# Performance work log

Measured on AMD Instinct MI355X. Metric: run time of the kernel, lower is better.

Reference implementation:

```python
import jax, jax.numpy as jnp
import numpy as np

B, T, TRAIN = 4, 2048, 1536
D, H, L, FF, V = 512, 8, 12, 2048, 100
DH = D // H
ROPE_BASE = 100000.0


def layer_norm(x, g, b, eps=1e-5):
    mu = jnp.mean(x, axis=-1, keepdims=True)
    var = jnp.mean(jnp.square(x - mu), axis=-1, keepdims=True)
    return (x - mu) * jax.lax.rsqrt(var + eps) * g + b


def rope_cos_sin(t, dh):
    inv_freq = 1.0 / (ROPE_BASE ** (jnp.arange(0, dh, 2, dtype=jnp.float32) / dh))  # (dh/2,)
    ang = jnp.arange(t, dtype=jnp.float32)[:, None] * inv_freq[None, :]  # (T, dh/2)
    return jnp.cos(ang), jnp.sin(ang)


def apply_rope_interleaved(x, cos, sin):
    # x: (B, T, H, DH); interleaved pairs (x0,x1),(x2,x3),...
    x1, x2 = x[..., 0::2], x[..., 1::2]
    c, s = cos[None, :, None, :], sin[None, :, None, :]
    r1 = x1 * c - x2 * s
    r2 = x1 * s + x2 * c
    return jnp.stack([r1, r2], axis=-1).reshape(x.shape)


def setup_inputs() -> dict:
    key = jax.random.key(0)
    ks = jax.random.split(key, 20)
    sc = 0.02
    inp = {
        'R': jax.random.normal(ks[0], (B, T, D), jnp.float32),
        'y_train': jax.random.randint(ks[1], (B, TRAIN), 0, V),
        'emb': jax.random.normal(ks[2], (V, D), jnp.float32) * sc,
        'Wqkv': jax.random.normal(ks[3], (L, D, 3 * D), jnp.float32) * sc,
        'bqkv': jnp.zeros((L, 3 * D), jnp.float32),
        'Wo': jax.random.normal(ks[4], (L, D, D), jnp.float32) * sc,
        'bo': jnp.zeros((L, D), jnp.float32),
        'ln1_g': jnp.ones((L, D), jnp.float32),
        'ln1_b': jnp.zeros((L, D), jnp.float32),
        'ln2_g': jnp.ones((L, D), jnp.float32),
        'ln2_b': jnp.zeros((L, D), jnp.float32),
        'W1': jax.random.normal(ks[5], (L, D, FF), jnp.float32) * sc,
        'b1': jnp.zeros((L, FF), jnp.float32),
        'W2': jax.random.normal(ks[6], (L, FF, D), jnp.float32) * sc,
        'b2': jnp.zeros((L, D), jnp.float32),
        'pW1': jax.random.normal(ks[7], (D, 2 * D), jnp.float32) * sc,
        'pb1': jnp.zeros((2 * D,), jnp.float32),
        'pW2': jax.random.normal(ks[8], (2 * D, V), jnp.float32) * sc,
        'pb2': jnp.zeros((V,), jnp.float32),
    }
    return inp


def icl_forward(R, y_train, emb, Wqkv, bqkv, Wo, bo, ln1_g, ln1_b, ln2_g, ln2_b, W1, b1, W2, b2, pW1, pb1, pW2, pb2):
    b, t, d = R.shape
    train = y_train.shape[1]
    # label embedding: train rows get emb[y], test rows get zeros
    y_emb = jnp.concatenate([emb[y_train], jnp.zeros((b, t - train, d), R.dtype)], axis=1)
    rep = R + y_emb
    # ICL mask: column j visible iff j < train or j == i
    idx = jnp.arange(t)
    allowed = (idx[None, :] < train) | (idx[:, None] == idx[None, :])
    mask = jnp.where(allowed, 0.0, -jnp.inf).astype(R.dtype)  # (T, T)
    cos, sin = rope_cos_sin(t, DH)
    scale = 1.0 / jnp.sqrt(jnp.asarray(DH, R.dtype))

    def block(x, p):
        wqkv, bq, wo, bob, g1, be1, g2, be2, w1, bb1, w2, bb2 = p
        h = layer_norm(x, g1, be1)
        qkv = h @ wqkv + bq  # (B,T,3D)
        q, k, v = jnp.split(qkv, 3, axis=-1)
        q = q.reshape(b, t, H, DH)
        k = k.reshape(b, t, H, DH)
        v = v.reshape(b, t, H, DH)
        q = apply_rope_interleaved(q, cos, sin)
        k = apply_rope_interleaved(k, cos, sin)
        scores = jnp.einsum('bthd,bshd->bhts', q, k) * scale + mask
        attn = jax.nn.softmax(scores, axis=-1)
        o = jnp.einsum('bhts,bshd->bthd', attn, v).reshape(b, t, d)
        x = x + o @ wo + bob
        h2 = layer_norm(x, g2, be2)
        x = x + jax.nn.gelu(h2 @ w1 + bb1) @ w2 + bb2
        return x, None

    rep, _ = jax.lax.scan(block, rep, (Wqkv, bqkv, Wo, bo, ln1_g, ln1_b, ln2_g, ln2_b, W1, b1, W2, b2))
    test = rep[:, train:, :]
    logits = jax.nn.gelu(test @ pW1 + pb1) @ pW2 + pb2  # (B, test, V)
    return logits


def reference(R, y_train, emb, Wqkv, bqkv, Wo, bo, ln1_g, ln1_b, ln2_g, ln2_b, W1, b1, W2, b2, pW1, pb1, pW2, pb2):
    return icl_forward(R, y_train, emb, Wqkv, bqkv, Wo, bo, ln1_g, ln1_b, ln2_g, ln2_b, W1, b1, W2, b2, pW1, pb1, pW2, pb2)
```

## Files before the change

### kernel.cpp

```cpp
#include <hip/hip_runtime.h>
#include <hip/hip_bf16.h>

#define BB 4
#define TT 2048
#define TRAIN 1536
#define DD 512
#define HH 8
#define LL 12
#define FFD 2048
#define VV 100
#define DH 64
#define NT (BB*TT)
#define NTEST (BB*(TT-TRAIN))

typedef __bf16 bf16x8 __attribute__((ext_vector_type(8)));
typedef float  f32x4  __attribute__((ext_vector_type(4)));
typedef unsigned int u32x4 __attribute__((ext_vector_type(4)));

#define GLDS16(g, l) __builtin_amdgcn_global_load_lds( \
    (const __attribute__((address_space(1))) void*)(g), \
    (__attribute__((address_space(3))) void*)(l), 16, 0, 0)

__global__ __launch_bounds__(256) void emb_add(const float* __restrict__ R,
                                               const int* __restrict__ y,
                                               const float* __restrict__ emb,
                                               float* __restrict__ rep) {
    int idx = blockIdx.x * 256 + threadIdx.x;
    int d = idx & 511;
    int n = idx >> 9;
    int t = n & (TT - 1);
    int b = n >> 11;
    float val = R[idx];
    if (t < TRAIN) {
        int tok = y[b * TRAIN + t];
        val += emb[(size_t)tok * DD + d];
    }
    rep[idx] = val;
}

__global__ __launch_bounds__(256) void ln_wave(const float* __restrict__ x,
                                               const float* __restrict__ g,
                                               const float* __restrict__ bta,
                                               __bf16* __restrict__ out) {
    int row = blockIdx.x * 4 + (threadIdx.x >> 6);
    int lane = threadIdx.x & 63;
    const float* xr = x + (size_t)row * DD + lane * 8;
    float4 a = *(const float4*)xr;
    float4 c = *(const float4*)(xr + 4);
    float s  = a.x + a.y + a.z + a.w + c.x + c.y + c.z + c.w;
    float sq = a.x*a.x + a.y*a.y + a.z*a.z + a.w*a.w + c.x*c.x + c.y*c.y + c.z*c.z + c.w*c.w;
#pragma unroll
    for (int off = 1; off < 64; off <<= 1) {
        s  += __shfl_xor(s, off);
        sq += __shfl_xor(sq, off);
    }
    float mu  = s * (1.0f / DD);
    float var = sq * (1.0f / DD) - mu * mu;
    float inv = rsqrtf(var + 1e-5f);
    const float* gp = g + lane * 8;
    const float* bp = bta + lane * 8;
    float4 g0 = *(const float4*)gp, g1 = *(const float4*)(gp + 4);
    float4 b0 = *(const float4*)bp, b1 = *(const float4*)(bp + 4);
    __bf16 o8[8];
    o8[0] = (__bf16)((a.x - mu) * inv * g0.x + b0.x);
    o8[1] = (__bf16)((a.y - mu) * inv * g0.y + b0.y);
    o8[2] = (__bf16)((a.z - mu) * inv * g0.z + b0.z);
    o8[3] = (__bf16)((a.w - mu) * inv * g0.w + b0.w);
    o8[4] = (__bf16)((c.x - mu) * inv * g1.x + b1.x);
    o8[5] = (__bf16)((c.y - mu) * inv * g1.y + b1.y);
    o8[6] = (__bf16)((c.z - mu) * inv * g1.z + b1.z);
    o8[7] = (__bf16)((c.w - mu) * inv * g1.w + b1.w);
    *(uint4*)(out + (size_t)row * DD + lane * 8) = *(uint4*)o8;
}

__global__ __launch_bounds__(256) void rope_tab(float* __restrict__ ctab, float* __restrict__ stab) {
    int idx = blockIdx.x * 256 + threadIdx.x;
    int p = idx & 31, t = idx >> 5;
    double freq = exp(-((double)(2 * p) / 64.0) * log(100000.0));
    double ang = (double)t * freq;
    ctab[idx] = (float)cos(ang);
    stab[idx] = (float)sin(ang);
}

__global__ __launch_bounds__(256) void rope_vt(const __bf16* __restrict__ qkv,
                                               const float* __restrict__ ctab,
                                               const float* __restrict__ stab,
                                               __bf16* __restrict__ qo,
                                               __bf16* __restrict__ ko,
                                               __bf16* __restrict__ vt) {
    int bh = blockIdx.y; int b = bh >> 3, h = bh & 7;
    int t0 = blockIdx.x * 64;
    __shared__ __bf16 tile[64][72];
    int tid = threadIdx.x;
    {
        int r = tid >> 2, cg = (tid & 3) * 16;
        const __bf16* src = qkv + (size_t)(b * TT + t0 + r) * (3 * DD) + 2 * DD + h * DH + cg;
        *(uint4*)&tile[r][cg]     = *(const uint4*)&src[0];
        *(uint4*)&tile[r][cg + 8] = *(const uint4*)&src[8];
    }
#pragma unroll
    for (int c = 0; c < 2; ++c) {
        int lin = c * 256 + tid;
        int tl = lin >> 3, u = lin & 7;
        int t = t0 + tl;
        const __bf16* base = qkv + (size_t)(b * TT + t) * (3 * DD) + h * DH + u * 8;
        uint4 qu = *(const uint4*)base;
        uint4 ku = *(const uint4*)(base + DD);
        float4 cv = *(const float4*)(ctab + t * 32 + u * 4);
        float4 sv = *(const float4*)(stab + t * 32 + u * 4);
        const __bf16* qp = (const __bf16*)&qu;
        const __bf16* kp = (const __bf16*)&ku;
        float cc[4] = {cv.x, cv.y, cv.z, cv.w};
        float ss[4] = {sv.x, sv.y, sv.z, sv.w};
        __bf16 oq[8], ok8[8];
#pragma unroll
        for (int j = 0; j < 4; ++j) {
            float x1 = (float)qp[2 * j], x2 = (float)qp[2 * j + 1];
            float k1 = (float)kp[2 * j], k2 = (float)kp[2 * j + 1];
            oq[2 * j]     = (__bf16)((x1 * cc[j] - x2 * ss[j]) * 0.125f);
            oq[2 * j + 1] = (__bf16)((x1 * ss[j] + x2 * cc[j]) * 0.125f);
            ok8[2 * j]     = (__bf16)(k1 * cc[j] - k2 * ss[j]);
            ok8[2 * j + 1] = (__bf16)(k1 * ss[j] + k2 * cc[j]);
        }
        size_t ob = ((size_t)bh * TT + t) * DH + u * 8;
        *(uint4*)(qo + ob) = *(uint4*)oq;
        *(uint4*)(ko + ob) = *(uint4*)ok8;
    }
    __syncthreads();
    {
        int dh = tid >> 2, tg = (tid & 3) * 16;
        __bf16 outv[16];
#pragma unroll
        for (int j = 0; j < 16; ++j) outv[j] = tile[tg + j][dh];
        __bf16* dst = vt + ((size_t)bh * DH + dh) * TT + t0 + tg;
        *(uint4*)&dst[0] = *(uint4*)&outv[0];
        *(uint4*)&dst[8] = *(uint4*)&outv[8];
    }
}

#define NCH (TRAIN/128)

__global__ __launch_bounds__(256, 2) void attn_mfma(const __bf16* __restrict__ q,
                                                    const __bf16* __restrict__ k,
                                                    const __bf16* __restrict__ vt,
                                                    __bf16* __restrict__ obuf) {
    __shared__ __align__(16) __bf16 Kb[2][128 * 64];
    __shared__ __align__(16) __bf16 Vb[2][64 * 128];
    __shared__ float sself[128];

    const int tid = threadIdx.x;
    const int lin = blockIdx.x;
    const int xcd = lin & 7, sblk = lin >> 3;
    const int bh = xcd * 4 + (sblk & 3);
    const int t0q = (sblk >> 2) * 128;
    const int b = bh >> 3, hh = bh & 7;
    const size_t kbase = (size_t)bh * TT * DH;
    const int w = tid >> 6;
    const int lane = tid & 63;
    const int l16 = lane & 15;
    const int quad = lane >> 4;
    const int x7 = l16 & 7;

    bf16x8 qa[2][2];
#pragma unroll
    for (int mi = 0; mi < 2; ++mi)
#pragma unroll
        for (int ks = 0; ks < 2; ++ks) {
            const __bf16* qg = q + kbase + (size_t)(t0q + w * 32 + mi * 16 + l16) * DH + ks * 32 + quad * 8;
            qa[mi][ks] = *(const bf16x8*)qg;
        }

    const int krl = lane >> 3, ksl = lane & 7;
    const int vrl = lane >> 4, vsl = lane & 15;

    f32x4 oa[2][4] = {};
    float lsum[2] = {0.f, 0.f};

    {
#pragma unroll
        for (int c = 0; c < 4; ++c) {
            int rb = w * 4 + c;
            GLDS16(k + kbase + (size_t)(rb * 8 + krl) * DH + ((ksl ^ krl) * 8), &Kb[0][rb * 512]);
            int dh = rb * 4 + vrl;
            GLDS16(vt + kbase + (size_t)dh * TT + ((vsl ^ (dh & 7)) * 8), &Vb[0][rb * 512]);
        }
    }

    for (int ci = 0; ci < NCH; ++ci) {
        __syncthreads();
        if (ci + 1 < NCH) {
            const __bf16* gk = k + kbase + (size_t)((ci + 1) * 128) * DH;
            __bf16* dK = Kb[(ci + 1) & 1];
            __bf16* dV = Vb[(ci + 1) & 1];
#pragma unroll
            for (int c = 0; c < 4; ++c) {
                int rb = w * 4 + c;
                GLDS16(gk + (size_t)(rb * 8 + krl) * DH + ((ksl ^ krl) * 8), dK + rb * 512);
                int dh = rb * 4 + vrl;
                GLDS16(vt + kbase + (size_t)dh * TT + (ci + 1) * 128 + ((vsl ^ (dh & 7)) * 8), dV + rb * 512);
            }
        }

        const __bf16* kc = Kb[ci & 1];
        f32x4 acc[2][8] = {};
        __builtin_amdgcn_s_setprio(1);
#pragma unroll
        for (int ks = 0; ks < 2; ++ks) {
            bf16x8 kf[8];
#pragma unroll
            for (int ni = 0; ni < 8; ++ni)
                kf[ni] = *(const bf16x8*)&kc[(ni * 16 + l16) * 64 + (((ks * 4 + quad) ^ x7) * 8)];
#pragma unroll
            for (int ni = 0; ni < 8; ++ni) {
                acc[0][ni] = __builtin_amdgcn_mfma_f32_16x16x32_bf16(kf[ni], qa[0][ks], acc[0][ni], 0, 0, 0);
                acc[1][ni] = __builtin_amdgcn_mfma_f32_16x16x32_bf16(kf[ni], qa[1][ks], acc[1][ni], 0, 0, 0);
            }
        }
        __builtin_amdgcn_s_setprio(0);

        u32x4 pa[2][4];
#pragma unroll
        for (int mi = 0; mi < 2; ++mi) {
            unsigned int pk[8][2];
            float rs = 0.f;
#pragma unroll
            for (int ni = 0; ni < 8; ++ni) {
                float p0 = __expf(acc[mi][ni][0]);
                float p1 = __expf(acc[mi][ni][1]);
                float p2 = __expf(acc[mi][ni][2]);
                float p3 = __expf(acc[mi][ni][3]);
                rs += (p0 + p1) + (p2 + p3);
                asm("v_cvt_pk_bf16_f32 %0, %1, %2" : "=v"(pk[ni][0]) : "v"(p0), "v"(p1));
                asm("v_cvt_pk_bf16_f32 %0, %1, %2" : "=v"(pk[ni][1]) : "v"(p2), "v"(p3));
            }
            rs += __shfl_xor(rs, 16);
            rs += __shfl_xor(rs, 32);
            lsum[mi] += rs;
#pragma unroll
            for (int ks = 0; ks < 4; ++ks)
#pragma unroll
                for (int rr = 0; rr < 2; ++rr) {
                    unsigned int A = pk[2 * ks][rr], Bv = pk[2 * ks + 1][rr];
                    asm("v_permlane32_swap_b32 %0, %1" : "+v"(A), "+v"(Bv));
                    asm("v_permlane16_swap_b32 %0, %1" : "+v"(A), "+v"(Bv));
                    pa[mi][ks][rr]     = A;
                    pa[mi][ks][rr + 2] = Bv;
                }
        }

        const __bf16* vc = Vb[ci & 1];
        __builtin_amdgcn_s_setprio(1);
#pragma unroll
        for (int ks = 0; ks < 4; ++ks) {
            bf16x8 vf[4];
#pragma unroll
            for (int ni = 0; ni < 4; ++ni)
                vf[ni] = *(const bf16x8*)&vc[(ni * 16 + l16) * 128 + (((ks * 4 + quad) ^ x7) * 8)];
            bf16x8 pa0, pa1;
            { u32x4 t = pa[0][ks]; __builtin_memcpy(&pa0, &t, 16); }
            { u32x4 t = pa[1][ks]; __builtin_memcpy(&pa1, &t, 16); }
#pragma unroll
            for (int ni = 0; ni < 4; ++ni) {
                oa[0][ni] = __builtin_amdgcn_mfma_f32_16x16x32_bf16(pa0, vf[ni], oa[0][ni], 0, 0, 0);
                oa[1][ni] = __builtin_amdgcn_mfma_f32_16x16x32_bf16(pa1, vf[ni], oa[1][ni], 0, 0, 0);
            }
        }
        __builtin_amdgcn_s_setprio(0);
    }

    float lr[2][4];
#pragma unroll
    for (int mi = 0; mi < 2; ++mi)
#pragma unroll
        for (int r = 0; r < 4; ++r)
            lr[mi][r] = __shfl(lsum[mi], quad * 4 + r);

    if (t0q >= TRAIN) {
        __syncthreads();
        {
            int dh = tid >> 2, cg = (tid & 3) * 32;
            const __bf16* vg = vt + kbase + (size_t)dh * TT + t0q + cg;
#pragma unroll
            for (int u = 0; u < 4; ++u)
                *(uint4*)&Vb[0][dh * 128 + cg + u * 8] = *(const uint4*)&vg[u * 8];
            int row = tid >> 1, hf = tid & 1;
            const __bf16* qp = q + kbase + (size_t)(t0q + row) * DH + hf * 32;
            const __bf16* kp = k + kbase + (size_t)(t0q + row) * DH + hf * 32;
            float dacc = 0.f;
#pragma unroll
            for (int u = 0; u < 4; ++u) {
                uint4 uq = *(const uint4*)&qp[u * 8];
                uint4 uk = *(const uint4*)&kp[u * 8];
                const __bf16* pq = (const __bf16*)&uq;
                const __bf16* pk2 = (const __bf16*)&uk;
#pragma unroll
                for (int j = 0; j < 8; ++j) dacc += (float)pq[j] * (float)pk2[j];
            }
            dacc += __shfl_xor(dacc, 1);
            sself[row] = dacc;
        }
        __syncthreads();
#pragma unroll
        for (int mi = 0; mi < 2; ++mi)
#pragma unroll
            for (int r = 0; r < 4; ++r) {
                int qr = w * 32 + mi * 16 + quad * 4 + r;
                float pp = __expf(sself[qr]);
                lr[mi][r] += pp;
#pragma unroll
                for (int ni = 0; ni < 4; ++ni)
                    oa[mi][ni][r] += pp * (float)Vb[0][(ni * 16 + l16) * 128 + qr];
            }
    }

#pragma unroll
    for (int mi = 0; mi < 2; ++mi)
#pragma unroll
        for (int r = 0; r < 4; ++r) {
            float inv = 1.f / lr[mi][r];
            int trow = t0q + w * 32 + mi * 16 + quad * 4 + r;
            __bf16* op = obuf + ((size_t)(b * TT) + trow) * DD + hh * 64;
#pragma unroll
            for (int ni = 0; ni < 4; ++ni)
                op[ni * 16 + l16] = (__bf16)(oa[mi][ni][r] * inv);
        }
}

__global__ __launch_bounds__(256) void transpose_pad(const float* __restrict__ src,
                                                     __bf16* __restrict__ dst,
                                                     int K, int N) {
    __shared__ __bf16 t[32][33];
    int n0 = blockIdx.x * 32, k0 = blockIdx.y * 32;
    int tx = threadIdx.x & 31, ty = threadIdx.x >> 5;
#pragma unroll
    for (int i = 0; i < 4; ++i) {
        int nn = n0 + tx;
        t[ty + i * 8][tx] = (nn < N) ? (__bf16)src[(size_t)(k0 + ty + i * 8) * N + nn] : (__bf16)0.f;
    }
    __syncthreads();
#pragma unroll
    for (int i = 0; i < 4; ++i) {
        dst[(size_t)(n0 + ty + i * 8) * K + k0 + tx] = t[tx][ty + i * 8];
    }
}

__global__ __launch_bounds__(256) void transpose_all(const float* __restrict__ s0,
                                                     const float* __restrict__ s1,
                                                     const float* __restrict__ s2,
                                                     const float* __restrict__ s3,
                                                     __bf16* __restrict__ d0, __bf16* __restrict__ d1,
                                                     __bf16* __restrict__ d2, __bf16* __restrict__ d3) {
    int i = blockIdx.x;
    const float* src; __bf16* dst; int K, N, tx, ty;
    if (i < 768)       { src = s0; dst = d0; K = 512;  N = 1536; int j = i;        tx = j % 48; ty = j / 48; }
    else if (i < 1024) { src = s1; dst = d1; K = 512;  N = 512;  int j = i - 768;  tx = j % 16; ty = j / 16; }
    else if (i < 2048) { src = s2; dst = d2; K = 512;  N = 2048; int j = i - 1024; tx = j % 64; ty = j / 64; }
    else               { src = s3; dst = d3; K = 2048; N = 512;  int j = i - 2048; tx = j % 16; ty = j / 16; }
    __shared__ __bf16 t[32][33];
    int n0 = tx * 32, k0 = ty * 32;
    int lx = threadIdx.x & 31, ly = threadIdx.x >> 5;
#pragma unroll
    for (int c = 0; c < 4; ++c)
        t[ly + c * 8][lx] = (__bf16)src[(size_t)(k0 + ly + c * 8) * N + n0 + lx];
    __syncthreads();
#pragma unroll
    for (int c = 0; c < 4; ++c)
        dst[(size_t)(n0 + ly + c * 8) * K + k0 + lx] = t[lx][ly + c * 8];
}

template <int EP, int TN>
__global__ __launch_bounds__(256) void gemm_bt(const __bf16* __restrict__ A,
                                               const __bf16* __restrict__ Bt,
                                               const float* __restrict__ bias,
                                               float* __restrict__ resid,
                                               __bf16* __restrict__ Cout,
                                               int M, int N, int K) {
    constexpr int NI = TN / 32;
    __shared__ __align__(16) __bf16 As[2][128 * 32];
    __shared__ __align__(16) __bf16 Bs[2][TN * 32];
    const int tid = threadIdx.x;
    const int gx = gridDim.x;
    const int linb = blockIdx.x + gx * blockIdx.y;
    const int xs = gx >> 3;
    const int xcd = linb & 7, sb = linb >> 3;
    const int bx = xcd * xs + (sb % xs);
    const int by = sb / xs;
    const int m0 = bx * 128;
    const int n0 = by * TN;
    const int lane = tid & 63;
    const int w = tid >> 6;
    const int wm = (w >> 1) * 64, wn = (w & 1) * (TN / 2);
    const int lrow = lane & 15;
    const int kq = (lane >> 4) * 8;

    f32x4 acc[4][NI] = {};

    const int srA = w * 32 + (lane >> 2);
    const int srB = w * (TN / 4) + (lane >> 2);
    const int scol = (lane & 3) * 8;
    const __bf16* gA = A  + (size_t)(m0 + srA) * K + scol;
    const __bf16* gB = Bt + (size_t)(n0 + srB) * K + scol;
    __bf16* lA0 = &As[0][(w * 32) * 32];
    __bf16* lA0b = lA0 + 16 * 32;
    __bf16* lA1 = &As[1][(w * 32) * 32];
    __bf16* lA1b = lA1 + 16 * 32;
    __bf16* lB0 = &Bs[0][(w * (TN / 4)) * 32];
    __bf16* lB1 = &Bs[1][(w * (TN / 4)) * 32];

    const int nk = K >> 6;
    for (int kt = 0; kt < nk; ++kt) {
        const int k0 = kt << 6;
        GLDS16(gA + k0,            lA0);
        GLDS16(gA + 16 * K + k0,   lA0b);
        GLDS16(gA + k0 + 32,       lA1);
        GLDS16(gA + 16 * K + k0 + 32, lA1b);
        GLDS16(gB + k0,            lB0);
        GLDS16(gB + k0 + 32,       lB1);
        if constexpr (TN == 128) {
            GLDS16(gB + 16 * K + k0,      lB0 + 16 * 32);
            GLDS16(gB + 16 * K + k0 + 32, lB1 + 16 * 32);
        }
        __syncthreads();
#pragma unroll
        for (int ps = 0; ps < 2; ++ps) {
            bf16x8 afr[4], bfr[NI];
#pragma unroll
            for (int i = 0; i < 4; ++i)
                afr[i] = *(const bf16x8*)&As[ps][(wm + i * 16 + lrow) * 32 + kq];
#pragma unroll
            for (int i = 0; i < NI; ++i)
                bfr[i] = *(const bf16x8*)&Bs[ps][(wn + i * 16 + lrow) * 32 + kq];
#pragma unroll
            for (int mi = 0; mi < 4; ++mi)
#pragma unroll
                for (int ni = 0; ni < NI; ++ni)
                    acc[mi][ni] = __builtin_amdgcn_mfma_f32_16x16x32_bf16(afr[mi], bfr[ni], acc[mi][ni], 0, 0, 0);
        }
        __syncthreads();
    }

    const int crow = (lane >> 4) * 4;
    const int ccol = lane & 15;
#pragma unroll
    for (int mi = 0; mi < 4; ++mi) {
#pragma unroll
        for (int ni = 0; ni < NI; ++ni) {
            int gn = n0 + wn + ni * 16 + ccol;
            float bv = bias[gn];
#pragma unroll
            for (int r = 0; r < 4; ++r) {
                int gm = m0 + wm + mi * 16 + crow + r;
                float vvv = acc[mi][ni][r] + bv;
                if constexpr (EP == 1) {
                    float x = vvv;
                    vvv = x / (1.f + __expf(-1.5957691216f * (x + 0.044715f * x * x * x)));
                }
                if constexpr (EP == 2) {
                    resid[(size_t)gm * N + gn] += vvv;
                } else if constexpr (EP == 4) {
                    if (gn < VV) resid[(size_t)gm * VV + gn] = vvv;
                } else {
                    Cout[(size_t)gm * N + gn] = (__bf16)vvv;
                }
            }
        }
    }
}

__global__ __launch_bounds__(256) void cast_test(const float* __restrict__ rep, __bf16* __restrict__ testb) {
    int idx = blockIdx.x * 256 + threadIdx.x;
    int d = idx & 511;
    int i = idx >> 9;
    int ttk = i & 511;
    int b = i >> 9;
    testb[idx] = (__bf16)rep[(size_t)(b * TT + TRAIN + ttk) * DD + d];
}

__global__ void pad_bias(const float* __restrict__ pb2, float* __restrict__ pb2p) {
    int t = threadIdx.x;
    if (t < 128) pb2p[t] = (t < VV) ? pb2[t] : 0.f;
}

extern "C" void kernel_launch(void* const* d_in, const int* in_sizes, int n_in,
                              void* d_out, int out_size, void* d_ws, size_t ws_size,
                              hipStream_t stream) {
    const float* R    = (const float*)d_in[0];
    const int*   y    = (const int*)d_in[1];
    const float* emb  = (const float*)d_in[2];
    const float* Wqkv = (const float*)d_in[3];
    const float* bqkv = (const float*)d_in[4];
    const float* Wo   = (const float*)d_in[5];
    const float* bo   = (const float*)d_in[6];
    const float* ln1g = (const float*)d_in[7];
    const float* ln1b = (const float*)d_in[8];
    const float* ln2g = (const float*)d_in[9];
    const float* ln2b = (const float*)d_in[10];
    const float* W1   = (const float*)d_in[11];
    const float* b1   = (const float*)d_in[12];
    const float* W2   = (const float*)d_in[13];
    const float* b2   = (const float*)d_in[14];
    const float* pW1  = (const float*)d_in[15];
    const float* pb1  = (const float*)d_in[16];
    const float* pW2  = (const float*)d_in[17];
    const float* pb2  = (const float*)d_in[18];

    char* p = (char*)d_ws;
    float* rep    = (float*)p;  p += (size_t)NT * DD * 4;
    __bf16* hbuf  = (__bf16*)p; p += (size_t)NT * DD * 2;
    __bf16* qkv   = (__bf16*)p;
    __bf16* ffb   = qkv;        p += (size_t)NT * FFD * 2;
    __bf16* qb    = (__bf16*)p; p += (size_t)NT * DD * 2;
    __bf16* kb    = (__bf16*)p; p += (size_t)NT * DD * 2;
    __bf16* vtb   = (__bf16*)p; p += (size_t)NT * DD * 2;
    __bf16* obuf  = (__bf16*)p; p += (size_t)NT * DD * 2;
    __bf16* wqkvT = (__bf16*)p; p += (size_t)1536 * 512 * 2;
    __bf16* woT   = (__bf16*)p; p += (size_t)512 * 512 * 2;
    __bf16* w1T   = (__bf16*)p; p += (size_t)2048 * 512 * 2;
    __bf16* w2T   = (__bf16*)p; p += (size_t)512 * 2048 * 2;
    float* ctab   = (float*)p;  p += (size_t)TT * 32 * 4;
    float* stab   = (float*)p;  p += (size_t)TT * 32 * 4;
    float* pb2p   = (float*)p;  p += 512;
    __bf16* testb = hbuf;
    __bf16* hb    = obuf;

    emb_add<<<NT * DD / 256, 256, 0, stream>>>(R, y, emb, rep);
    rope_tab<<<TT * 32 / 256, 256, 0, stream>>>(ctab, stab);

    for (int l = 0; l < LL; ++l) {
        ln_wave<<<NT / 4, 256, 0, stream>>>(rep, ln1g + l * DD, ln1b + l * DD, hbuf);
        transpose_all<<<3072, 256, 0, stream>>>(Wqkv + (size_t)l * DD * 3 * DD, Wo + (size_t)l * DD * DD,
                                                W1 + (size_t)l * DD * FFD, W2 + (size_t)l * FFD * DD,
                                                wqkvT, woT, w1T, w2T);
        gemm_bt<0, 128><<<dim3(NT / 128, 1536 / 128), 256, 0, stream>>>(hbuf, wqkvT, bqkv + l * 3 * DD, nullptr, qkv, NT, 3 * DD, DD);
        rope_vt<<<dim3(TT / 64, BB * HH), 256, 0, stream>>>(qkv, ctab, stab, qb, kb, vtb);
        attn_mfma<<<dim3(512), 256, 0, stream>>>(qb, kb, vtb, obuf);
        gemm_bt<2, 64><<<dim3(NT / 128, 512 / 64), 256, 0, stream>>>(obuf, woT, bo + l * DD, rep, nullptr, NT, DD, DD);
        ln_wave<<<NT / 4, 256, 0, stream>>>(rep, ln2g + l * DD, ln2b + l * DD, hbuf);
        gemm_bt<1, 128><<<dim3(NT / 128, FFD / 128), 256, 0, stream>>>(hbuf, w1T, b1 + l * FFD, nullptr, ffb, NT, FFD, DD);
        gemm_bt<2, 64><<<dim3(NT / 128, 512 / 64), 256, 0, stream>>>(ffb, w2T, b2 + l * DD, rep, nullptr, NT, DD, FFD);
    }

    cast_test<<<NTEST * DD / 256, 256, 0, stream>>>(rep, testb);
    transpose_pad<<<dim3(1024 / 32, 512 / 32), 256, 0, stream>>>(pW1, w1T, DD, 2 * DD);
    gemm_bt<1, 64><<<dim3(NTEST / 128, 1024 / 64), 256, 0, stream>>>(testb, w1T, pb1, nullptr, hb, NTEST, 2 * DD, DD);
    pad_bias<<<1, 128, 0, stream>>>(pb2, pb2p);
    transpose_pad<<<dim3(128 / 32, 1024 / 32), 256, 0, stream>>>(pW2, w2T, 2 * DD, VV);
    gemm_bt<4, 128><<<dim3(NTEST / 128, 1), 256, 0, stream>>>(hb, w2T, pb2p, (float*)d_out, nullptr, NTEST, 128, 2 * DD);
}
```

Before: 2.295 ms.

## Double-buffer GEMM K tiles with XOR-swizzled LDS and larger N tiles

```diff
diff --git a/kernel.cpp b/kernel.cpp
--- a/kernel.cpp
+++ b/kernel.cpp
@@ -369,15 +369,16 @@
 }
 
 template <int EP, int TN>
-__global__ __launch_bounds__(256) void gemm_bt(const __bf16* __restrict__ A,
-                                               const __bf16* __restrict__ Bt,
-                                               const float* __restrict__ bias,
-                                               float* __restrict__ resid,
-                                               __bf16* __restrict__ Cout,
-                                               int M, int N, int K) {
+__global__ __launch_bounds__(256, 2) void gemm_bt(const __bf16* __restrict__ A,
+                                                  const __bf16* __restrict__ Bt,
+                                                  const float* __restrict__ bias,
+                                                  float* __restrict__ resid,
+                                                  __bf16* __restrict__ Cout,
+                                                  int M, int N, int K) {
     constexpr int NI = TN / 32;
-    __shared__ __align__(16) __bf16 As[2][128 * 32];
-    __shared__ __align__(16) __bf16 Bs[2][TN * 32];
+    constexpr int BC = TN / 32;
+    __shared__ __align__(16) __bf16 As[2][128 * 64];
+    __shared__ __align__(16) __bf16 Bs[2][TN * 64];
     const int tid = threadIdx.x;
     const int gx = gridDim.x;
     const int linb = blockIdx.x + gx * blockIdx.y;
@@ -391,52 +392,48 @@
     const int w = tid >> 6;
     const int wm = (w >> 1) * 64, wn = (w & 1) * (TN / 2);
     const int lrow = lane & 15;
-    const int kq = (lane >> 4) * 8;
+    const int quad = lane >> 4;
+    const int x7 = lrow & 7;
 
     f32x4 acc[4][NI] = {};
 
-    const int srA = w * 32 + (lane >> 2);
-    const int srB = w * (TN / 4) + (lane >> 2);
-    const int scol = (lane & 3) * 8;
-    const __bf16* gA = A  + (size_t)(m0 + srA) * K + scol;
-    const __bf16* gB = Bt + (size_t)(n0 + srB) * K + scol;
-    __bf16* lA0 = &As[0][(w * 32) * 32];
-    __bf16* lA0b = lA0 + 16 * 32;
-    __bf16* lA1 = &As[1][(w * 32) * 32];
-    __bf16* lA1b = lA1 + 16 * 32;
-    __bf16* lB0 = &Bs[0][(w * (TN / 4)) * 32];
-    __bf16* lB1 = &Bs[1][(w * (TN / 4)) * 32];
+    const int sr = lane >> 3;
+    const int sc = ((lane & 7) ^ sr) * 8;
+    const __bf16* gA = A  + (size_t)(m0 + w * 32 + sr) * K + sc;
+    const __bf16* gB = Bt + (size_t)(n0 + w * (TN / 4) + sr) * K + sc;
+
+    auto stage = [&](int kt, int buf) {
+        const int k0 = kt << 6;
+#pragma unroll
+        for (int c = 0; c < 4; ++c)
+            GLDS16(gA + (size_t)(c * 8) * K + k0, &As[buf][(w * 32 + c * 8) * 64]);
+#pragma unroll
+        for (int c = 0; c < BC; ++c)
+            GLDS16(gB + (size_t)(c * 8) * K + k0, &Bs[buf][(w * (TN / 4) + c * 8) * 64]);
+    };
 
     const int nk = K >> 6;
+    stage(0, 0);
     for (int kt = 0; kt < nk; ++kt) {
-        const int k0 = kt << 6;
-        GLDS16(gA + k0,            lA0);
-        GLDS16(gA + 16 * K + k0,   lA0b);
-        GLDS16(gA + k0 + 32,       lA1);
-        GLDS16(gA + 16 * K + k0 + 32, lA1b);
-        GLDS16(gB + k0,            lB0);
-        GLDS16(gB + k0 + 32,       lB1);
-        if constexpr (TN == 128) {
-            GLDS16(gB + 16 * K + k0,      lB0 + 16 * 32);
-            GLDS16(gB + 16 * K + k0 + 32, lB1 + 16 * 32);
-        }
         __syncthreads();
-#pragma unroll
-        for (int ps = 0; ps < 2; ++ps) {
+        if (kt + 1 < nk) stage(kt + 1, (kt + 1) & 1);
+        const __bf16* as = As[kt & 1];
+        const __bf16* bs = Bs[kt & 1];
+#pragma unroll
+        for (int ks = 0; ks < 2; ++ks) {
             bf16x8 afr[4], bfr[NI];
 #pragma unroll
             for (int i = 0; i < 4; ++i)
-                afr[i] = *(const bf16x8*)&As[ps][(wm + i * 16 + lrow) * 32 + kq];
+                afr[i] = *(const bf16x8*)&as[(wm + i * 16 + lrow) * 64 + (((ks * 4 + quad) ^ x7) * 8)];
 #pragma unroll
             for (int i = 0; i < NI; ++i)
-                bfr[i] = *(const bf16x8*)&Bs[ps][(wn + i * 16 + lrow) * 32 + kq];
+                bfr[i] = *(const bf16x8*)&bs[(wn + i * 16 + lrow) * 64 + (((ks * 4 + quad) ^ x7) * 8)];
 #pragma unroll
             for (int mi = 0; mi < 4; ++mi)
 #pragma unroll
                 for (int ni = 0; ni < NI; ++ni)
                     acc[mi][ni] = __builtin_amdgcn_mfma_f32_16x16x32_bf16(afr[mi], bfr[ni], acc[mi][ni], 0, 0, 0);
         }
-        __syncthreads();
     }
 
     const int crow = (lane >> 4) * 4;
@@ -534,10 +531,10 @@
         gemm_bt<0, 128><<<dim3(NT / 128, 1536 / 128), 256, 0, stream>>>(hbuf, wqkvT, bqkv + l * 3 * DD, nullptr, qkv, NT, 3 * DD, DD);
         rope_vt<<<dim3(TT / 64, BB * HH), 256, 0, stream>>>(qkv, ctab, stab, qb, kb, vtb);
         attn_mfma<<<dim3(512), 256, 0, stream>>>(qb, kb, vtb, obuf);
-        gemm_bt<2, 64><<<dim3(NT / 128, 512 / 64), 256, 0, stream>>>(obuf, woT, bo + l * DD, rep, nullptr, NT, DD, DD);
+        gemm_bt<2, 128><<<dim3(NT / 128, 512 / 128), 256, 0, stream>>>(obuf, woT, bo + l * DD, rep, nullptr, NT, DD, DD);
         ln_wave<<<NT / 4, 256, 0, stream>>>(rep, ln2g + l * DD, ln2b + l * DD, hbuf);
         gemm_bt<1, 128><<<dim3(NT / 128, FFD / 128), 256, 0, stream>>>(hbuf, w1T, b1 + l * FFD, nullptr, ffb, NT, FFD, DD);
-        gemm_bt<2, 64><<<dim3(NT / 128, 512 / 64), 256, 0, stream>>>(ffb, w2T, b2 + l * DD, rep, nullptr, NT, DD, FFD);
+        gemm_bt<2, 128><<<dim3(NT / 128, 512 / 128), 256, 0, stream>>>(ffb, w2T, b2 + l * DD, rep, nullptr, NT, DD, FFD);
     }
 
     cast_test<<<NTEST * DD / 256, 256, 0, stream>>>(rep, testb);
```

Measured after the change: 2.494 ms. 1.09x slower.

## Halve attention query tile to 64 rows and single-buffer V for more occupancy

Applied to the files above, without the earlier changes.

```diff
diff --git a/kernel.cpp b/kernel.cpp
--- a/kernel.cpp
+++ b/kernel.cpp
@@ -140,19 +140,19 @@
 
 #define NCH (TRAIN/128)
 
-__global__ __launch_bounds__(256, 2) void attn_mfma(const __bf16* __restrict__ q,
+__global__ __launch_bounds__(256, 3) void attn_mfma(const __bf16* __restrict__ q,
                                                     const __bf16* __restrict__ k,
                                                     const __bf16* __restrict__ vt,
                                                     __bf16* __restrict__ obuf) {
     __shared__ __align__(16) __bf16 Kb[2][128 * 64];
-    __shared__ __align__(16) __bf16 Vb[2][64 * 128];
-    __shared__ float sself[128];
+    __shared__ __align__(16) __bf16 Vb[64 * 128];
+    __shared__ float sself[64];
 
     const int tid = threadIdx.x;
     const int lin = blockIdx.x;
     const int xcd = lin & 7, sblk = lin >> 3;
     const int bh = xcd * 4 + (sblk & 3);
-    const int t0q = (sblk >> 2) * 128;
+    const int t0q = (sblk >> 2) * 64;
     const int b = bh >> 3, hh = bh & 7;
     const size_t kbase = (size_t)bh * TT * DH;
     const int w = tid >> 6;
@@ -161,48 +161,38 @@
     const int quad = lane >> 4;
     const int x7 = l16 & 7;
 
-    bf16x8 qa[2][2];
-#pragma unroll
-    for (int mi = 0; mi < 2; ++mi)
-#pragma unroll
-        for (int ks = 0; ks < 2; ++ks) {
-            const __bf16* qg = q + kbase + (size_t)(t0q + w * 32 + mi * 16 + l16) * DH + ks * 32 + quad * 8;
-            qa[mi][ks] = *(const bf16x8*)qg;
-        }
+    bf16x8 qa[2];
+#pragma unroll
+    for (int ks = 0; ks < 2; ++ks) {
+        const __bf16* qg = q + kbase + (size_t)(t0q + w * 16 + l16) * DH + ks * 32 + quad * 8;
+        qa[ks] = *(const bf16x8*)qg;
+    }
 
     const int krl = lane >> 3, ksl = lane & 7;
     const int vrl = lane >> 4, vsl = lane & 15;
 
-    f32x4 oa[2][4] = {};
-    float lsum[2] = {0.f, 0.f};
+    f32x4 oa[4] = {};
+    float lsum = 0.f;
 
     {
 #pragma unroll
         for (int c = 0; c < 4; ++c) {
             int rb = w * 4 + c;
             GLDS16(k + kbase + (size_t)(rb * 8 + krl) * DH + ((ksl ^ krl) * 8), &Kb[0][rb * 512]);
-            int dh = rb * 4 + vrl;
-            GLDS16(vt + kbase + (size_t)dh * TT + ((vsl ^ (dh & 7)) * 8), &Vb[0][rb * 512]);
         }
     }
 
     for (int ci = 0; ci < NCH; ++ci) {
         __syncthreads();
-        if (ci + 1 < NCH) {
-            const __bf16* gk = k + kbase + (size_t)((ci + 1) * 128) * DH;
-            __bf16* dK = Kb[(ci + 1) & 1];
-            __bf16* dV = Vb[(ci + 1) & 1];
-#pragma unroll
-            for (int c = 0; c < 4; ++c) {
-                int rb = w * 4 + c;
-                GLDS16(gk + (size_t)(rb * 8 + krl) * DH + ((ksl ^ krl) * 8), dK + rb * 512);
-                int dh = rb * 4 + vrl;
-                GLDS16(vt + kbase + (size_t)dh * TT + (ci + 1) * 128 + ((vsl ^ (dh & 7)) * 8), dV + rb * 512);
-            }
+#pragma unroll
+        for (int c = 0; c < 4; ++c) {
+            int rb = w * 4 + c;
+            int dh = rb * 4 + vrl;
+            GLDS16(vt + kbase + (size_t)dh * TT + ci * 128 + ((vsl ^ (dh & 7)) * 8), &Vb[rb * 512]);
         }
 
         const __bf16* kc = Kb[ci & 1];
-        f32x4 acc[2][8] = {};
+        f32x4 acc[8] = {};
         __builtin_amdgcn_s_setprio(1);
 #pragma unroll
         for (int ks = 0; ks < 2; ++ks) {
@@ -211,31 +201,28 @@
             for (int ni = 0; ni < 8; ++ni)
                 kf[ni] = *(const bf16x8*)&kc[(ni * 16 + l16) * 64 + (((ks * 4 + quad) ^ x7) * 8)];
 #pragma unroll
-            for (int ni = 0; ni < 8; ++ni) {
-                acc[0][ni] = __builtin_amdgcn_mfma_f32_16x16x32_bf16(kf[ni], qa[0][ks], acc[0][ni], 0, 0, 0);
-                acc[1][ni] = __builtin_amdgcn_mfma_f32_16x16x32_bf16(kf[ni], qa[1][ks], acc[1][ni], 0, 0, 0);
-            }
+            for (int ni = 0; ni < 8; ++ni)
+                acc[ni] = __builtin_amdgcn_mfma_f32_16x16x32_bf16(kf[ni], qa[ks], acc[ni], 0, 0, 0);
         }
         __builtin_amdgcn_s_setprio(0);
 
-        u32x4 pa[2][4];
-#pragma unroll
-        for (int mi = 0; mi < 2; ++mi) {
+        u32x4 pa[4];
+        {
             unsigned int pk[8][2];
             float rs = 0.f;
 #pragma unroll
             for (int ni = 0; ni < 8; ++ni) {
-                float p0 = __expf(acc[mi][ni][0]);
-                float p1 = __expf(acc[mi][ni][1]);
-                float p2 = __expf(acc[mi][ni][2]);
-                float p3 = __expf(acc[mi][ni][3]);
+                float p0 = __expf(acc[ni][0]);
+                float p1 = __expf(acc[ni][1]);
+                float p2 = __expf(acc[ni][2]);
+                float p3 = __expf(acc[ni][3]);
                 rs += (p0 + p1) + (p2 + p3);
                 asm("v_cvt_pk_bf16_f32 %0, %1, %2" : "=v"(pk[ni][0]) : "v"(p0), "v"(p1));
                 asm("v_cvt_pk_bf16_f32 %0, %1, %2" : "=v"(pk[ni][1]) : "v"(p2), "v"(p3));
             }
             rs += __shfl_xor(rs, 16);
             rs += __shfl_xor(rs, 32);
-            lsum[mi] += rs;
+            lsum += rs;
 #pragma unroll
             for (int ks = 0; ks < 4; ++ks)
 #pragma unroll
@@ -243,37 +230,42 @@
                     unsigned int A = pk[2 * ks][rr], Bv = pk[2 * ks + 1][rr];
                     asm("v_permlane32_swap_b32 %0, %1" : "+v"(A), "+v"(Bv));
                     asm("v_permlane16_swap_b32 %0, %1" : "+v"(A), "+v"(Bv));
-                    pa[mi][ks][rr]     = A;
-                    pa[mi][ks][rr + 2] = Bv;
+                    pa[ks][rr]     = A;
+                    pa[ks][rr + 2] = Bv;
                 }
         }
 
-        const __bf16* vc = Vb[ci & 1];
+        __syncthreads();
+        if (ci + 1 < NCH) {
+            const __bf16* gk = k + kbase + (size_t)((ci + 1) * 128) * DH;
+            __bf16* dst = Kb[(ci + 1) & 1];
+#pragma unroll
+            for (int c = 0; c < 4; ++c) {
+                int rb = w * 4 + c;
+                GLDS16(gk + (size_t)(rb * 8 + krl) * DH + ((ksl ^ krl) * 8), dst + rb * 512);
+            }
+        }
+
         __builtin_amdgcn_s_setprio(1);
 #pragma unroll
         for (int ks = 0; ks < 4; ++ks) {
             bf16x8 vf[4];
 #pragma unroll
             for (int ni = 0; ni < 4; ++ni)
-                vf[ni] = *(const bf16x8*)&vc[(ni * 16 + l16) * 128 + (((ks * 4 + quad) ^ x7) * 8)];
-            bf16x8 pa0, pa1;
-            { u32x4 t = pa[0][ks]; __builtin_memcpy(&pa0, &t, 16); }
-            { u32x4 t = pa[1][ks]; __builtin_memcpy(&pa1, &t, 16); }
-#pragma unroll
-            for (int ni = 0; ni < 4; ++ni) {
-                oa[0][ni] = __builtin_amdgcn_mfma_f32_16x16x32_bf16(pa0, vf[ni], oa[0][ni], 0, 0, 0);
-                oa[1][ni] = __builtin_amdgcn_mfma_f32_16x16x32_bf16(pa1, vf[ni], oa[1][ni], 0, 0, 0);
-            }
+                vf[ni] = *(const bf16x8*)&Vb[(ni * 16 + l16) * 128 + (((ks * 4 + quad) ^ x7) * 8)];
+            bf16x8 pa0;
+            { u32x4 t = pa[ks]; __builtin_memcpy(&pa0, &t, 16); }
+#pragma unroll
+            for (int ni = 0; ni < 4; ++ni)
+                oa[ni] = __builtin_amdgcn_mfma_f32_16x16x32_bf16(pa0, vf[ni], oa[ni], 0, 0, 0);
         }
         __builtin_amdgcn_s_setprio(0);
     }
 
-    float lr[2][4];
-#pragma unroll
-    for (int mi = 0; mi < 2; ++mi)
-#pragma unroll
-        for (int r = 0; r < 4; ++r)
-            lr[mi][r] = __shfl(lsum[mi], quad * 4 + r);
+    float lr[4];
+#pragma unroll
+    for (int r = 0; r < 4; ++r)
+        lr[r] = __shfl(lsum, quad * 4 + r);
 
     if (t0q >= TRAIN) {
         __syncthreads();
@@ -282,13 +274,13 @@
             const __bf16* vg = vt + kbase + (size_t)dh * TT + t0q + cg;
 #pragma unroll
             for (int u = 0; u < 4; ++u)
-                *(uint4*)&Vb[0][dh * 128 + cg + u * 8] = *(const uint4*)&vg[u * 8];
-            int row = tid >> 1, hf = tid & 1;
-            const __bf16* qp = q + kbase + (size_t)(t0q + row) * DH + hf * 32;
-            const __bf16* kp = k + kbase + (size_t)(t0q + row) * DH + hf * 32;
+                *(uint4*)&Vb[dh * 128 + cg + u * 8] = *(const uint4*)&vg[u * 8];
+            int row = tid >> 2, part = tid & 3;
+            const __bf16* qp = q + kbase + (size_t)(t0q + row) * DH + part * 16;
+            const __bf16* kp = k + kbase + (size_t)(t0q + row) * DH + part * 16;
             float dacc = 0.f;
 #pragma unroll
-            for (int u = 0; u < 4; ++u) {
+            for (int u = 0; u < 2; ++u) {
                 uint4 uq = *(const uint4*)&qp[u * 8];
                 uint4 uk = *(const uint4*)&kp[u * 8];
                 const __bf16* pq = (const __bf16*)&uq;
@@ -297,33 +289,30 @@
                 for (int j = 0; j < 8; ++j) dacc += (float)pq[j] * (float)pk2[j];
             }
             dacc += __shfl_xor(dacc, 1);
+            dacc += __shfl_xor(dacc, 2);
             sself[row] = dacc;
         }
         __syncthreads();
 #pragma unroll
-        for (int mi = 0; mi < 2; ++mi)
-#pragma unroll
-            for (int r = 0; r < 4; ++r) {
-                int qr = w * 32 + mi * 16 + quad * 4 + r;
-                float pp = __expf(sself[qr]);
-                lr[mi][r] += pp;
-#pragma unroll
-                for (int ni = 0; ni < 4; ++ni)
-                    oa[mi][ni][r] += pp * (float)Vb[0][(ni * 16 + l16) * 128 + qr];
-            }
-    }
-
-#pragma unroll
-    for (int mi = 0; mi < 2; ++mi)
-#pragma unroll
         for (int r = 0; r < 4; ++r) {
-            float inv = 1.f / lr[mi][r];
-            int trow = t0q + w * 32 + mi * 16 + quad * 4 + r;
-            __bf16* op = obuf + ((size_t)(b * TT) + trow) * DD + hh * 64;
+            int qr = w * 16 + quad * 4 + r;
+            float pp = __expf(sself[qr]);
+            lr[r] += pp;
 #pragma unroll
             for (int ni = 0; ni < 4; ++ni)
-                op[ni * 16 + l16] = (__bf16)(oa[mi][ni][r] * inv);
-        }
+                oa[ni][r] += pp * (float)Vb[(ni * 16 + l16) * 128 + qr];
+        }
+    }
+
+#pragma unroll
+    for (int r = 0; r < 4; ++r) {
+        float inv = 1.f / lr[r];
+        int trow = t0q + w * 16 + quad * 4 + r;
+        __bf16* op = obuf + ((size_t)(b * TT) + trow) * DD + hh * 64;
+#pragma unroll
+        for (int ni = 0; ni < 4; ++ni)
+            op[ni * 16 + l16] = (__bf16)(oa[ni][r] * inv);
+    }
 }
 
 __global__ __launch_bounds__(256) void transpose_pad(const float* __restrict__ src,
@@ -533,7 +522,7 @@
                                                 wqkvT, woT, w1T, w2T);
         gemm_bt<0, 128><<<dim3(NT / 128, 1536 / 128), 256, 0, stream>>>(hbuf, wqkvT, bqkv + l * 3 * DD, nullptr, qkv, NT, 3 * DD, DD);
         rope_vt<<<dim3(TT / 64, BB * HH), 256, 0, stream>>>(qkv, ctab, stab, qb, kb, vtb);
-        attn_mfma<<<dim3(512), 256, 0, stream>>>(qb, kb, vtb, obuf);
+        attn_mfma<<<dim3(1024), 256, 0, stream>>>(qb, kb, vtb, obuf);
         gemm_bt<2, 64><<<dim3(NT / 128, 512 / 64), 256, 0, stream>>>(obuf, woT, bo + l * DD, rep, nullptr, NT, DD, DD);
         ln_wave<<<NT / 4, 256, 0, stream>>>(rep, ln2g + l * DD, ln2b + l * DD, hbuf);
         gemm_bt<1, 128><<<dim3(NT / 128, FFD / 128), 256, 0, stream>>>(hbuf, w1T, b1 + l * FFD, nullptr, ffb, NT, FFD, DD);
```

After: 2.413 ms. +5.2%, slower.
